# Performance work log

Measured on AMD Instinct MI355X. Metric: run time of the kernel, lower is better.

## Reference

```python
import jax, jax.numpy as jnp
import numpy as np

T, B, DG, DH, S = 48, 96, 192, 384, 3
LAM, ETA = 0.9, 0.5
LN_EPS = 1e-5

def layernorm(x, g, b):
    m = jnp.mean(x, axis=-1, keepdims=True)
    v = jnp.var(x, axis=-1, keepdims=True)
    return (x - m) * jax.lax.rsqrt(v + LN_EPS) * g + b

def setup_inputs() -> dict:
    key = jax.random.key(0)
    k0, k1, k2, k3 = jax.random.split(key, 4)
    z_seq = jax.random.normal(k0, (T, B, DG), jnp.float32)
    # kaiming-uniform-ish / xavier-ish scaling for realism
    W_h = jax.random.normal(k1, (DH, DH), jnp.float32) * (2.0 / DH) ** 0.5
    W_g = jax.random.normal(k2, (DH, DG), jnp.float32) * (1.0 / DG) ** 0.5
    b_h = jnp.zeros((DH,), jnp.float32)
    ln_g = jnp.ones((DH,), jnp.float32)
    ln_b = jnp.zeros((DH,), jnp.float32)
    alpha_fw = jax.random.uniform(k3, (1,), jnp.float32)  # cfg.alpha_fw (learned scalar)
    return dict(z_seq=z_seq, W_h=W_h, W_g=W_g, b_h=b_h, ln_g=ln_g, ln_b=ln_b, alpha_fw=alpha_fw)

def reference(z_seq, W_h, W_g, b_h, ln_g, ln_b, alpha_fw):
    # compute_k(): curvature of cosine gate
    k = jnp.where(alpha_fw >= 0,
                  1.0 + jax.nn.softplus(alpha_fw),
                  1.0 / (1.0 + jax.nn.softplus(-alpha_fw)))  # shape (1,)

    def step(carry, z_t):
        h, A = carry                                   # h: [B,DH], A: [B,DH,DH]
        h_base = h @ W_h.T + z_t @ W_g.T + b_h          # [B,DH]
        h_s = jax.nn.relu(layernorm(h_base, ln_g, ln_b))
        # inner fast-weight settling loop with cosine-similarity gate
        for _ in range(S):
            Ah = jnp.einsum('bij,bj->bi', A, h_s)       # bmm(A, h)
            dot = jnp.sum(h_s * Ah, axis=-1, keepdims=True)
            n1 = jnp.maximum(jnp.linalg.norm(h_s, axis=-1, keepdims=True), 1e-6)
            n2 = jnp.maximum(jnp.linalg.norm(Ah, axis=-1, keepdims=True), 1e-6)
            R = jnp.clip(dot / (n1 * n2), 0.0, 1.0)
            a = 1.0 - (1.0 - R) ** k                    # alpha_dyn, [B,1]
            h_s = jax.nn.relu(layernorm((1.0 - a * a) * h_base + a * Ah, ln_g, ln_b))
        h = h_s
        # Hebbian fast-weight update: A <- lambda*A + eta * h h^T
        A = LAM * A + ETA * jnp.einsum('bi,bj->bij', h, h)
        return (h, A), None

    Bn, Dh = z_seq.shape[1], W_h.shape[0]
    h0 = jnp.zeros((Bn, Dh), z_seq.dtype)
    A0 = jnp.zeros((Bn, Dh, Dh), z_seq.dtype)
    (h, A), _ = jax.lax.scan(step, (h0, A0), z_seq[:-1])

    # final (query) step: no gating, no A update, h_s = relu(LN(h_base + A h_s))
    z_t = z_seq[-1]
    h_base = h @ W_h.T + z_t @ W_g.T + b_h
    h = jax.nn.relu(layernorm(h_base, ln_g, ln_b))
    for _ in range(S):
        Ah = jnp.einsum('bij,bj->bi', A, h)
        h = jax.nn.relu(layernorm(h_base + Ah, ln_g, ln_b))
    return h
```

## Files before the change

kernel.cpp:

```cpp
#include <hip/hip_runtime.h>
#include <math.h>

#define TT    48
#define BB    96
#define DG    192
#define DH    384
#define NSTEP 47
#define SETI  3
#define NT    512
#define NWAVE 8
#define NOW   6
#define NG    32
#define RPG   12
#define LWROWS 192
#define LWSTR  97
#define PNT   256
#define PTT   24

typedef unsigned short ushort_t;
typedef float f32x2 __attribute__((ext_vector_type(2)));

template <int CTRL, int RM>
__device__ __forceinline__ float dppadd(float acc, float x) {
  int t = __builtin_amdgcn_update_dpp(0, __float_as_int(x), CTRL, RM, 0xF, false);
  return acc + __int_as_float(t);
}

__device__ __forceinline__ float row16_sum(float v) {
  v = dppadd<0x128, 0xF>(v, v);
  v = dppadd<0x124, 0xF>(v, v);
  v = dppadd<0x122, 0xF>(v, v);
  v = dppadd<0x121, 0xF>(v, v);
  return v;
}

__device__ __forceinline__ float wave_sum63(float v) {
  v = row16_sum(v);
  v = dppadd<0x142, 0xA>(v, v);
  v = dppadd<0x143, 0xC>(v, v);
  return v;
}

__device__ __forceinline__ float blo(unsigned u) {
  return __uint_as_float(u << 16);
}
__device__ __forceinline__ float bhi(unsigned u) {
  return __uint_as_float(u & 0xFFFF0000u);
}
__device__ __forceinline__ f32x2 pkfma(f32x2 a, f32x2 b, f32x2 c) {
  return __builtin_elementwise_fma(a, b, c);
}

__device__ __forceinline__ float rowdot(const uint2* w, const f32x2 (&h2)[12]) {
  f32x2 a0 = {0.f, 0.f}, a1 = {0.f, 0.f};
#pragma unroll
  for (int c = 0; c < 6; ++c) {
    uint2 u = w[c];
    a0 = pkfma(f32x2{blo(u.x), bhi(u.x)}, h2[2 * c], a0);
    a1 = pkfma(f32x2{blo(u.y), bhi(u.y)}, h2[2 * c + 1], a1);
  }
  return row16_sum((a0.x + a1.x) + (a0.y + a1.y));
}

__device__ __forceinline__ void matvec_full(
    const uint2* __restrict__ lwh, const ushort_t* __restrict__ Wh_b,
    const float* __restrict__ hs, const float* __restrict__ gzs,
    float* __restrict__ hbs, float& s1, float& s2,
    int g, int lane16, bool with_h)
{
  float rs[RPG];
  if (with_h) {
    const uint2* wsrc = (const uint2*)Wh_b;
    uint2 uw0[12];
#pragma unroll
    for (int pp = 0; pp < 2; ++pp)
#pragma unroll
      for (int c = 0; c < 6; ++c)
        uw0[pp * 6 + c] =
            wsrc[(size_t)(g + NG * (6 + pp)) * (DH / 4) + lane16 + 16 * c];
    f32x2 h2[12];
    const float4* h4 = (const float4*)hs;
#pragma unroll
    for (int c = 0; c < 6; ++c) {
      float4 hh = h4[lane16 + 16 * c];
      h2[2 * c]     = f32x2{hh.x, hh.y};
      h2[2 * c + 1] = f32x2{hh.z, hh.w};
    }
    uint2 uw1[12];
#pragma unroll
    for (int pp = 0; pp < 2; ++pp)
#pragma unroll
      for (int c = 0; c < 6; ++c)
        uw1[pp * 6 + c] =
            wsrc[(size_t)(g + NG * (8 + pp)) * (DH / 4) + lane16 + 16 * c];
#pragma unroll
    for (int p = 0; p < 6; ++p) {
      const int r = g + NG * p;
      f32x2 a0 = {0.f, 0.f}, a1 = {0.f, 0.f};
#pragma unroll
      for (int c = 0; c < 6; ++c) {
        uint2 u = lwh[r * LWSTR + lane16 + 16 * c];
        a0 = pkfma(f32x2{blo(u.x), bhi(u.x)}, h2[2 * c], a0);
        a1 = pkfma(f32x2{blo(u.y), bhi(u.y)}, h2[2 * c + 1], a1);
      }
      rs[p] = row16_sum((a0.x + a1.x) + (a0.y + a1.y));
    }
    rs[6] = rowdot(uw0, h2);
    rs[7] = rowdot(uw0 + 6, h2);
    uint2 uw2[12];
#pragma unroll
    for (int pp = 0; pp < 2; ++pp)
#pragma unroll
      for (int c = 0; c < 6; ++c)
        uw2[pp * 6 + c] =
            wsrc[(size_t)(g + NG * (10 + pp)) * (DH / 4) + lane16 + 16 * c];
    rs[8] = rowdot(uw1, h2);
    rs[9] = rowdot(uw1 + 6, h2);
    rs[10] = rowdot(uw2, h2);
    rs[11] = rowdot(uw2 + 6, h2);
  } else {
#pragma unroll
    for (int p = 0; p < RPG; ++p) rs[p] = 0.f;
  }
  if (lane16 == 0) {
#pragma unroll
    for (int p = 0; p < RPG; ++p) {
      const int r = g + NG * p;
      float vv = rs[p] + gzs[r];
      hbs[r] = vv;
      s1 += vv;
      s2 += vv * vv;
    }
  }
}

__device__ __forceinline__ void matvec_ref(
    const float* __restrict__ Wh_f, const float* __restrict__ Wg_f,
    const float* __restrict__ hs, const float* __restrict__ zsh,
    const float (&bias)[RPG], float* __restrict__ hbs,
    float& s1, float& s2, int g, int lane16, bool with_h)
{
  f32x2 h2[12];
  if (with_h) {
    const float4* h4 = (const float4*)hs;
#pragma unroll
    for (int c = 0; c < 6; ++c) {
      float4 hh = h4[lane16 + 16 * c];
      h2[2 * c]     = f32x2{hh.x, hh.y};
      h2[2 * c + 1] = f32x2{hh.z, hh.w};
    }
  }
  float4 zz[3];
  const float4* z4 = (const float4*)zsh;
#pragma unroll
  for (int c = 0; c < 3; ++c) zz[c] = z4[lane16 + 16 * c];
#pragma unroll 2
  for (int p = 0; p < RPG; ++p) {
    const int r = g + NG * p;
    f32x2 a0 = {0.f, 0.f}, a1 = {0.f, 0.f};
    const float4* wg = (const float4*)Wg_f + (size_t)r * (DG / 4);
#pragma unroll
    for (int c = 0; c < 3; ++c) {
      float4 w = wg[lane16 + 16 * c];
      a0 = pkfma(f32x2{w.x, w.y}, f32x2{zz[c].x, zz[c].y}, a0);
      a1 = pkfma(f32x2{w.z, w.w}, f32x2{zz[c].z, zz[c].w}, a1);
    }
    if (with_h) {
      const float4* wh = (const float4*)Wh_f + (size_t)r * (DH / 4);
#pragma unroll
      for (int c = 0; c < 6; ++c) {
        float4 w = wh[lane16 + 16 * c];
        a0 = pkfma(f32x2{w.x, w.y}, h2[2 * c], a0);
        a1 = pkfma(f32x2{w.z, w.w}, h2[2 * c + 1], a1);
      }
    }
    float acc = row16_sum((a0.x + a1.x) + (a0.y + a1.y));
    if (lane16 == 0) {
      float vv = acc + bias[p];
      hbs[r] = vv;
      s1 += vv;
      s2 += vv * vv;
    }
  }
}

template <bool FULL>
__global__ __launch_bounds__(NT, 2) void fw_rnn_kernel(
    const float* __restrict__ z_seq,
    const float* __restrict__ Wh_f,
    const float* __restrict__ Wg_f,
    const ushort_t* __restrict__ Wh_b,
    const float* __restrict__ gz,
    const float* __restrict__ b_h,
    const float* __restrict__ ln_g,
    const float* __restrict__ ln_b,
    const float* __restrict__ alpha_fw,
    float* __restrict__ out)
{
  __shared__ __align__(16) uint2 lwh[LWROWS * LWSTR];
  __shared__ __align__(16) float hs[DH];
  __shared__ __align__(16) float hbs[DH];
  __shared__ __align__(16) float gzs[DH];
  __shared__ __align__(16) float zsh[DG];
  __shared__ float wlam[NSTEP];
  __shared__ __align__(16) float carr[48];
  __shared__ __align__(16) float redA[NWAVE * 2];
  __shared__ __align__(16) float redB[2][32];

  const int tid    = threadIdx.x;
  const int b      = blockIdx.x;
  const int lane   = tid & 63, wv = tid >> 6;
  const int g      = tid >> 4, lane16 = tid & 15;
  const bool owner = (tid < DH);
  const bool zst   = (!FULL) && (tid >= DH) && (tid < DH + DG / 4);

  if (FULL) {
    const uint2* src = (const uint2*)Wh_b;
    for (int i = tid; i < LWROWS * 96; i += NT) {
      int row = i / 96, col = i - 96 * (i / 96);
      lwh[row * LWSTR + col] = src[(size_t)row * 96 + col];
    }
  }

  float bias[RPG];
#pragma unroll
  for (int p = 0; p < RPG; ++p) bias[p] = 0.f;
  if (!FULL && lane16 == 0) {
#pragma unroll
    for (int p = 0; p < RPG; ++p) bias[p] = b_h[g + NG * p];
  }
  float g_i = 0.f, be_i = 0.f;
  if (owner) { g_i = ln_g[tid]; be_i = ln_b[tid]; }

  const float af   = alpha_fw[0];
  const float kcur = (af >= 0.f) ? (1.f + log1pf(expf(af)))
                                 : (1.f / (1.f + log1pf(expf(-af))));
  const float invD = 1.0f / (float)DH;

  float hcol[48];
#pragma unroll
  for (int q = 0; q < 48; ++q) hcol[q] = 0.f;
  float4 hregA[6], hregB[6];
#pragma unroll
  for (int c = 0; c < 6; ++c) {
    hregA[c] = float4{0.f, 0.f, 0.f, 0.f};
    hregB[c] = float4{0.f, 0.f, 0.f, 0.f};
  }

  if (FULL && tid < DH / 4)
    ((float4*)gzs)[tid] = ((const float4*)(gz + (size_t)b * DH))[tid];
  if (!FULL && tid < DG / 4)
    ((float4*)zsh)[tid] = ((const float4*)(z_seq + (size_t)b * DG))[tid];
  if (tid < 48) carr[tid] = 0.f;
  if (tid < 2) { redB[tid][30] = 0.f; redB[tid][31] = 0.f; }
  __syncthreads();

  float Shb = 0.f, Shb2 = 0.f;

  for (int t = 0; t < NSTEP; ++t) {
    float4 gzn = {0.f, 0.f, 0.f, 0.f};
    if (FULL && tid < DH / 4)
      gzn = ((const float4*)(gz + ((size_t)(t + 1) * BB + b) * DH))[tid];

    float s1 = 0.f, s2 = 0.f;
    if (FULL)
      matvec_full(lwh, Wh_b, hs, gzs, hbs, s1, s2, g, lane16, t > 0);
    else
      matvec_ref(Wh_f, Wg_f, hs, zsh, bias, hbs, s1, s2, g, lane16, t > 0);

    if (t > 0) {
      if (g == t - 1) {
#pragma unroll
        for (int c = 0; c < 6; ++c) hregA[c] = ((const float4*)hs)[lane16 + 16 * c];
      }
      if (g + NG == t - 1) {
#pragma unroll
        for (int c = 0; c < 6; ++c) hregB[c] = ((const float4*)hs)[lane16 + 16 * c];
      }
    }
    {
      float v0 = wave_sum63(s1);
      float v1 = wave_sum63(s2);
      if (lane == 63) { redA[wv * 2] = v0; redA[wv * 2 + 1] = v1; }
    }
    __syncthreads();

    float hb = 0.f, hsv = 0.f;
    if (owner) {
      float S1 = 0.f, S2 = 0.f;
      const float4* ra4 = (const float4*)redA;
#pragma unroll
      for (int q = 0; q < 4; ++q) {
        float4 ch = ra4[q];
        S1 += ch.x + ch.z;
        S2 += ch.y + ch.w;
      }
      Shb = S1; Shb2 = S2;
      hb = hbs[tid];
      float m   = S1 * invD;
      float var = S2 * invD - m * m;
      hsv = fmaxf((hb - m) * rsqrtf(var + 1e-5f) * g_i + be_i, 0.f);
      hs[tid] = hsv;
    }
    if (t == 0) {
      if (owner) hcol[0] = hsv;
      if (tid == 0) wlam[0] = 0.5f;
      if (FULL && tid < DH / 4) ((float4*)gzs)[tid] = gzn;
      if (zst)
        ((float4*)zsh)[tid - DH] =
            ((const float4*)(z_seq + ((size_t)1 * BB + b) * DG))[tid - DH];
      __syncthreads();
      continue;
    }
    __syncthreads();

    float4 znext;
    if (zst)
      znext = ((const float4*)(z_seq + ((size_t)(t + 1) * BB + b) * DG))[tid - DH];

    for (int s = 0; s < SETI; ++s) {
      if (g < t) {
        float4 ss[6];
        const float4* s4 = (const float4*)hs;
#pragma unroll
        for (int c = 0; c < 6; ++c) ss[c] = s4[lane16 + 16 * c];
        {
          f32x2 p0 = {0.f, 0.f}, p1 = {0.f, 0.f};
#pragma unroll
          for (int c = 0; c < 6; ++c) {
            p0 = pkfma(f32x2{hregA[c].x, hregA[c].y}, f32x2{ss[c].x, ss[c].y}, p0);
            p1 = pkfma(f32x2{hregA[c].z, hregA[c].w}, f32x2{ss[c].z, ss[c].w}, p1);
          }
          float p = row16_sum((p0.x + p1.x) + (p0.y + p1.y));
          if (lane16 == 0) carr[g] = p * wlam[g];
        }
        if (g + NG < t) {
          f32x2 p0 = {0.f, 0.f}, p1 = {0.f, 0.f};
#pragma unroll
          for (int c = 0; c < 6; ++c) {
            p0 = pkfma(f32x2{hregB[c].x, hregB[c].y}, f32x2{ss[c].x, ss[c].y}, p0);
            p1 = pkfma(f32x2{hregB[c].z, hregB[c].w}, f32x2{ss[c].z, ss[c].w}, p1);
          }
          float p = row16_sum((p0.x + p1.x) + (p0.y + p1.y));
          if (lane16 == 0) carr[g + NG] = p * wlam[g + NG];
        }
      }
      __syncthreads();

      float ah = 0.f;
      if (owner) {
        const float4* c4 = (const float4*)carr;
        float a0 = 0.f, a1 = 0.f, a2 = 0.f, a3 = 0.f;
#pragma unroll
        for (int q = 0; q < 12; ++q) {
          float4 cc = c4[q];
          a0 = fmaf(cc.x, hcol[4 * q + 0], a0);
          a1 = fmaf(cc.y, hcol[4 * q + 1], a1);
          a2 = fmaf(cc.z, hcol[4 * q + 2], a2);
          a3 = fmaf(cc.w, hcol[4 * q + 3], a3);
        }
        ah = (a0 + a2) + (a1 + a3);
        float v0 = wave_sum63(hsv * ah);
        float v1 = wave_sum63(hsv * hsv);
        float v2 = wave_sum63(ah * ah);
        float v3 = wave_sum63(hb * ah);
        float v4 = wave_sum63(ah);
        if (lane == 63) {
          float* rb = redB[s & 1];
          rb[wv * 5 + 0] = v0; rb[wv * 5 + 1] = v1; rb[wv * 5 + 2] = v2;
          rb[wv * 5 + 3] = v3; rb[wv * 5 + 4] = v4;
        }
      }
      __syncthreads();

      if (owner) {
        const float4* rb4 = (const float4*)redB[s & 1];
        float S[5] = {0.f, 0.f, 0.f, 0.f, 0.f};
#pragma unroll
        for (int q = 0; q < 8; ++q) {
          float4 ch = rb4[q];
          S[(4 * q + 0) % 5] += ch.x;
          S[(4 * q + 1) % 5] += ch.y;
          S[(4 * q + 2) % 5] += ch.z;
          S[(4 * q + 3) % 5] += ch.w;
        }
        float n1 = fmaxf(sqrtf(S[1]), 1e-6f);
        float n2 = fmaxf(sqrtf(S[2]), 1e-6f);
        float R  = fminf(fmaxf(__fdividef(S[0], n1 * n2), 0.f), 1.f);
        float a  = 1.f - __expf(kcur * __logf(1.f - R));
        float beta = 1.f - a * a;
        float mu  = (beta * Shb + a * S[4]) * invD;
        float Exx = (beta * beta * Shb2 + 2.f * beta * a * S[3] + a * a * S[2]) * invD;
        float var = Exx - mu * mu;
        float xv  = beta * hb + a * ah;
        hsv = fmaxf((xv - mu) * rsqrtf(var + 1e-5f) * g_i + be_i, 0.f);
        hs[tid] = hsv;
        if (s == SETI - 1) {
#pragma unroll
          for (int q = 0; q < 48; ++q)
            if (q == t) hcol[q] = hsv;
        }
      }
      if (s == SETI - 1) {
        if (tid < t) wlam[tid] *= 0.9f;
        else if (tid == t) wlam[tid] = 0.5f;
        if (FULL && tid < DH / 4) ((float4*)gzs)[tid] = gzn;
        if (zst) ((float4*)zsh)[tid - DH] = znext;
      }
      __syncthreads();
    }
  }

  {
    float s1 = 0.f, s2 = 0.f;
    if (FULL)
      matvec_full(lwh, Wh_b, hs, gzs, hbs, s1, s2, g, lane16, true);
    else
      matvec_ref(Wh_f, Wg_f, hs, zsh, bias, hbs, s1, s2, g, lane16, true);
    if (g + NG == NSTEP - 1) {
#pragma unroll
      for (int c = 0; c < 6; ++c) hregB[c] = ((const float4*)hs)[lane16 + 16 * c];
    }
    {
      float v0 = wave_sum63(s1);
      float v1 = wave_sum63(s2);
      if (lane == 63) { redA[wv * 2] = v0; redA[wv * 2 + 1] = v1; }
    }
    __syncthreads();

    float hb = 0.f, hv = 0.f;
    if (owner) {
      float S1 = 0.f, S2 = 0.f;
      const float4* ra4 = (const float4*)redA;
#pragma unroll
      for (int q = 0; q < 4; ++q) {
        float4 ch = ra4[q];
        S1 += ch.x + ch.z;
        S2 += ch.y + ch.w;
      }
      Shb = S1; Shb2 = S2;
      hb = hbs[tid];
      float m   = S1 * invD;
      float var = S2 * invD - m * m;
      hv = fmaxf((hb - m) * rsqrtf(var + 1e-5f) * g_i + be_i, 0.f);
      hs[tid] = hv;
    }
    __syncthreads();

    for (int s = 0; s < SETI; ++s) {
      {
        float4 ss[6];
        const float4* s4 = (const float4*)hs;
#pragma unroll
        for (int c = 0; c < 6; ++c) ss[c] = s4[lane16 + 16 * c];
        {
          f32x2 p0 = {0.f, 0.f}, p1 = {0.f, 0.f};
#pragma unroll
          for (int c = 0; c < 6; ++c) {
            p0 = pkfma(f32x2{hregA[c].x, hregA[c].y}, f32x2{ss[c].x, ss[c].y}, p0);
            p1 = pkfma(f32x2{hregA[c].z, hregA[c].w}, f32x2{ss[c].z, ss[c].w}, p1);
          }
          float p = row16_sum((p0.x + p1.x) + (p0.y + p1.y));
          if (lane16 == 0) carr[g] = p * wlam[g];
        }
        if (g + NG < NSTEP) {
          f32x2 p0 = {0.f, 0.f}, p1 = {0.f, 0.f};
#pragma unroll
          for (int c = 0; c < 6; ++c) {
            p0 = pkfma(f32x2{hregB[c].x, hregB[c].y}, f32x2{ss[c].x, ss[c].y}, p0);
            p1 = pkfma(f32x2{hregB[c].z, hregB[c].w}, f32x2{ss[c].z, ss[c].w}, p1);
          }
          float p = row16_sum((p0.x + p1.x) + (p0.y + p1.y));
          if (lane16 == 0) carr[g + NG] = p * wlam[g + NG];
        }
      }
      __syncthreads();

      float ah = 0.f;
      if (owner) {
        const float4* c4 = (const float4*)carr;
        float a0 = 0.f, a1 = 0.f, a2 = 0.f, a3 = 0.f;
#pragma unroll
        for (int q = 0; q < 12; ++q) {
          float4 cc = c4[q];
          a0 = fmaf(cc.x, hcol[4 * q + 0], a0);
          a1 = fmaf(cc.y, hcol[4 * q + 1], a1);
          a2 = fmaf(cc.z, hcol[4 * q + 2], a2);
          a3 = fmaf(cc.w, hcol[4 * q + 3], a3);
        }
        ah = (a0 + a2) + (a1 + a3);
        float v0 = wave_sum63(ah);
        float v1 = wave_sum63(ah * ah);
        float v2 = wave_sum63(hb * ah);
        if (lane == 63) {
          float* rb = redB[s & 1];
          rb[wv * 5 + 0] = v0; rb[wv * 5 + 1] = v1; rb[wv * 5 + 2] = v2;
        }
      }
      __syncthreads();

      if (owner) {
        const float4* rb4 = (const float4*)redB[s & 1];
        float S[5] = {0.f, 0.f, 0.f, 0.f, 0.f};
#pragma unroll
        for (int q = 0; q < 8; ++q) {
          float4 ch = rb4[q];
          S[(4 * q + 0) % 5] += ch.x;
          S[(4 * q + 1) % 5] += ch.y;
          S[(4 * q + 2) % 5] += ch.z;
          S[(4 * q + 3) % 5] += ch.w;
        }
        float Sx  = Shb + S[0];
        float Sxx = Shb2 + 2.f * S[2] + S[1];
        float mu  = Sx * invD;
        float var = Sxx * invD - mu * mu;
        float xv  = hb + ah;
        hv = fmaxf((xv - mu) * rsqrtf(var + 1e-5f) * g_i + be_i, 0.f);
        if (s < SETI - 1) hs[tid] = hv;
      }
      if (s < SETI - 1) __syncthreads();
    }

    if (owner) out[(size_t)b * DH + tid] = hv;
  }
}

__global__ __launch_bounds__(PNT) void prep_kernel(
    const float* __restrict__ z_seq, const float* __restrict__ Wg,
    const float* __restrict__ W_h, const float* __restrict__ b_h,
    ushort_t* __restrict__ Whb, float* __restrict__ gz)
{
  __shared__ __align__(16) float zsh[PTT * DG];
  const int tid = threadIdx.x, b = blockIdx.x;
  const int t0 = blockIdx.y * PTT;
  const int g = tid >> 4, lane16 = tid & 15;

  {
    int lid = ((blockIdx.y * BB + blockIdx.x) * PNT + tid) * 3;
#pragma unroll
    for (int k = 0; k < 3; ++k) {
      int idx = lid + k;
      if (idx < DH * DH) {
        unsigned u = __float_as_uint(W_h[idx]);
        unsigned r = (u + 0x7FFFu + ((u >> 16) & 1u)) >> 16;
        Whb[idx] = (ushort_t)r;
      }
    }
  }

  for (int i = tid; i < PTT * DG / 4; i += PNT) {
    int tt = i / (DG / 4), c = i - tt * (DG / 4);
    ((float4*)zsh)[i] =
        ((const float4*)(z_seq + ((size_t)(t0 + tt) * BB + b) * DG))[c];
  }
  __syncthreads();

  for (int pp = 0; pp < 3; ++pp) {
    const int rbase = 24 * g + 8 * pp;
    float4 w[24];
#pragma unroll
    for (int j = 0; j < 8; ++j)
#pragma unroll
      for (int c = 0; c < 3; ++c)
        w[j * 3 + c] =
            ((const float4*)Wg)[(size_t)(rbase + j) * (DG / 4) + lane16 + 16 * c];
    float4 bh0 = {0.f, 0.f, 0.f, 0.f}, bh1 = {0.f, 0.f, 0.f, 0.f};
    if (lane16 == 0) {
      bh0 = ((const float4*)b_h)[rbase / 4];
      bh1 = ((const float4*)b_h)[rbase / 4 + 1];
    }
    for (int tt = 0; tt < PTT; ++tt) {
      float4 zz[3];
#pragma unroll
      for (int c = 0; c < 3; ++c)
        zz[c] = ((const float4*)zsh)[tt * (DG / 4) + lane16 + 16 * c];
      float rs[8];
#pragma unroll
      for (int j = 0; j < 8; ++j) {
        f32x2 a0 = {0.f, 0.f}, a1 = {0.f, 0.f};
#pragma unroll
        for (int c = 0; c < 3; ++c) {
          a0 = pkfma(f32x2{w[j * 3 + c].x, w[j * 3 + c].y},
                     f32x2{zz[c].x, zz[c].y}, a0);
          a1 = pkfma(f32x2{w[j * 3 + c].z, w[j * 3 + c].w},
                     f32x2{zz[c].z, zz[c].w}, a1);
        }
        rs[j] = row16_sum((a0.x + a1.x) + (a0.y + a1.y));
      }
      if (lane16 == 0) {
        float* grow = gz + ((size_t)(t0 + tt) * BB + b) * DH + rbase;
        ((float4*)grow)[0] =
            float4{rs[0] + bh0.x, rs[1] + bh0.y, rs[2] + bh0.z, rs[3] + bh0.w};
        ((float4*)grow)[1] =
            float4{rs[4] + bh1.x, rs[5] + bh1.y, rs[6] + bh1.z, rs[7] + bh1.w};
      }
    }
  }
}

extern "C" void kernel_launch(void* const* d_in, const int* in_sizes, int n_in,
                              void* d_out, int out_size, void* d_ws, size_t ws_size,
                              hipStream_t stream) {
  const float* z_seq    = (const float*)d_in[0];
  const float* W_h      = (const float*)d_in[1];
  const float* W_g      = (const float*)d_in[2];
  const float* b_h      = (const float*)d_in[3];
  const float* ln_g     = (const float*)d_in[4];
  const float* ln_b     = (const float*)d_in[5];
  const float* alpha_fw = (const float*)d_in[6];
  float* out = (float*)d_out;

  const size_t nWh = (size_t)DH * DH;
  const size_t bf16Bytes = nWh * sizeof(ushort_t);
  const size_t gzBytes   = (size_t)TT * BB * DH * sizeof(float);

  if (ws_size >= bf16Bytes + gzBytes) {
    ushort_t* Whb = (ushort_t*)d_ws;
    float* gz = (float*)((char*)d_ws + bf16Bytes);
    prep_kernel<<<dim3(BB, 2), dim3(PNT), 0, stream>>>(
        z_seq, W_g, W_h, b_h, Whb, gz);
    fw_rnn_kernel<true><<<dim3(BB), dim3(NT), 0, stream>>>(
        z_seq, W_h, W_g, Whb, gz, b_h, ln_g, ln_b, alpha_fw, out);
  } else {
    fw_rnn_kernel<false><<<dim3(BB), dim3(NT), 0, stream>>>(
        z_seq, W_h, W_g, nullptr, nullptr, b_h, ln_g, ln_b, alpha_fw, out);
  }
}
```

Measured before the change: 529.3 us.

## Recompute settled hidden state redundantly per thread to drop barriers in gate loop

Instead of having owner threads write the normalized hidden state to shared memory and then barrier, each thread group now rebuilds h_s locally from h_base, the previous Ah (stored in a new shared array), and the LN gains, using gate scalars every thread computes from the reduction buffer. This removes one __syncthreads per settling iteration plus the one after the initial layernorm. The next z load is also hoisted to the top of the step. The cost is extra redundant ALU work and shared-memory reads (hbs, ahs, ln_g, ln_b) per iteration, and more registers.

```diff
diff --git a/kernel.cpp b/kernel.cpp
--- a/kernel.cpp
+++ b/kernel.cpp
@@ -9,7 +9,6 @@
 #define SETI  3
 #define NT    512
 #define NWAVE 8
-#define NOW   6
 #define NG    32
 #define RPG   12
 #define LWROWS 192
@@ -25,7 +24,6 @@
   int t = __builtin_amdgcn_update_dpp(0, __float_as_int(x), CTRL, RM, 0xF, false);
   return acc + __int_as_float(t);
 }
-
 __device__ __forceinline__ float row16_sum(float v) {
   v = dppadd<0x128, 0xF>(v, v);
   v = dppadd<0x124, 0xF>(v, v);
@@ -33,24 +31,17 @@
   v = dppadd<0x121, 0xF>(v, v);
   return v;
 }
-
 __device__ __forceinline__ float wave_sum63(float v) {
   v = row16_sum(v);
   v = dppadd<0x142, 0xA>(v, v);
   v = dppadd<0x143, 0xC>(v, v);
   return v;
 }
-
-__device__ __forceinline__ float blo(unsigned u) {
-  return __uint_as_float(u << 16);
-}
-__device__ __forceinline__ float bhi(unsigned u) {
-  return __uint_as_float(u & 0xFFFF0000u);
-}
+__device__ __forceinline__ float blo(unsigned u) { return __uint_as_float(u << 16); }
+__device__ __forceinline__ float bhi(unsigned u) { return __uint_as_float(u & 0xFFFF0000u); }
 __device__ __forceinline__ f32x2 pkfma(f32x2 a, f32x2 b, f32x2 c) {
   return __builtin_elementwise_fma(a, b, c);
 }
-
 __device__ __forceinline__ float rowdot(const uint2* w, const f32x2 (&h2)[12]) {
   f32x2 a0 = {0.f, 0.f}, a1 = {0.f, 0.f};
 #pragma unroll
@@ -60,6 +51,31 @@
     a1 = pkfma(f32x2{blo(u.y), bhi(u.y)}, h2[2 * c + 1], a1);
   }
   return row16_sum((a0.x + a1.x) + (a0.y + a1.y));
+}
+
+__device__ __forceinline__ void gate_from(
+    const float* __restrict__ rb, float Shb, float Shb2, float kcur, float invD,
+    float& aG, float& betaG, float& muG, float& rstdG, float& S2o)
+{
+  const float4* rb4 = (const float4*)rb;
+  float S[5] = {0.f, 0.f, 0.f, 0.f, 0.f};
+#pragma unroll
+  for (int q = 0; q < 8; ++q) {
+    float4 ch = rb4[q];
+    S[(4 * q + 0) % 5] += ch.x;
+    S[(4 * q + 1) % 5] += ch.y;
+    S[(4 * q + 2) % 5] += ch.z;
+    S[(4 * q + 3) % 5] += ch.w;
+  }
+  float n1 = fmaxf(sqrtf(S[1]), 1e-6f);
+  float n2 = fmaxf(sqrtf(S[2]), 1e-6f);
+  float R  = fminf(fmaxf(__fdividef(S[0], n1 * n2), 0.f), 1.f);
+  aG   = 1.f - __expf(kcur * __logf(1.f - R));
+  betaG = 1.f - aG * aG;
+  muG  = (betaG * Shb + aG * S[4]) * invD;
+  float Exx = (betaG * betaG * Shb2 + 2.f * betaG * aG * S[3] + aG * aG * S[2]) * invD;
+  rstdG = rsqrtf(Exx - muG * muG + 1e-5f);
+  S2o = S[2];
 }
 
 __device__ __forceinline__ void matvec_full(
@@ -200,6 +216,9 @@
   __shared__ __align__(16) uint2 lwh[LWROWS * LWSTR];
   __shared__ __align__(16) float hs[DH];
   __shared__ __align__(16) float hbs[DH];
+  __shared__ __align__(16) float ahs[DH];
+  __shared__ __align__(16) float lngs[DH];
+  __shared__ __align__(16) float lnbs[DH];
   __shared__ __align__(16) float gzs[DH];
   __shared__ __align__(16) float zsh[DG];
   __shared__ float wlam[NSTEP];
@@ -230,7 +249,10 @@
     for (int p = 0; p < RPG; ++p) bias[p] = b_h[g + NG * p];
   }
   float g_i = 0.f, be_i = 0.f;
-  if (owner) { g_i = ln_g[tid]; be_i = ln_b[tid]; }
+  if (owner) {
+    g_i = ln_g[tid]; be_i = ln_b[tid];
+    lngs[tid] = g_i; lnbs[tid] = be_i;
+  }
 
   const float af   = alpha_fw[0];
   const float kcur = (af >= 0.f) ? (1.f + log1pf(expf(af)))
@@ -261,6 +283,9 @@
     float4 gzn = {0.f, 0.f, 0.f, 0.f};
     if (FULL && tid < DH / 4)
       gzn = ((const float4*)(gz + ((size_t)(t + 1) * BB + b) * DH))[tid];
+    float4 znext;
+    if (zst)
+      znext = ((const float4*)(z_seq + ((size_t)(t + 1) * BB + b) * DG))[tid - DH];
 
     float s1 = 0.f, s2 = 0.f;
     if (FULL)
@@ -285,8 +310,7 @@
     }
     __syncthreads();
 
-    float hb = 0.f, hsv = 0.f;
-    if (owner) {
+    {
       float S1 = 0.f, S2 = 0.f;
       const float4* ra4 = (const float4*)redA;
 #pragma unroll
@@ -296,40 +320,67 @@
         S2 += ch.y + ch.w;
       }
       Shb = S1; Shb2 = S2;
-      hb = hbs[tid];
-      float m   = S1 * invD;
-      float var = S2 * invD - m * m;
-      hsv = fmaxf((hb - m) * rsqrtf(var + 1e-5f) * g_i + be_i, 0.f);
-      hs[tid] = hsv;
+    }
+    const float m0    = Shb * invD;
+    const float rstd0 = rsqrtf(Shb2 * invD - m0 * m0 + 1e-5f);
+
+    float hb = 0.f, hsv = 0.f, ah = 0.f;
+    if (owner) {
+      hb  = hbs[tid];
+      hsv = fmaxf((hb - m0) * rstd0 * g_i + be_i, 0.f);
     }
     if (t == 0) {
-      if (owner) hcol[0] = hsv;
+      if (owner) { hs[tid] = hsv; hcol[0] = hsv; }
       if (tid == 0) wlam[0] = 0.5f;
       if (FULL && tid < DH / 4) ((float4*)gzs)[tid] = gzn;
-      if (zst)
-        ((float4*)zsh)[tid - DH] =
-            ((const float4*)(z_seq + ((size_t)1 * BB + b) * DG))[tid - DH];
+      if (zst) ((float4*)zsh)[tid - DH] = znext;
       __syncthreads();
       continue;
     }
-    __syncthreads();
-
-    float4 znext;
-    if (zst)
-      znext = ((const float4*)(z_seq + ((size_t)(t + 1) * BB + b) * DG))[tid - DH];
-
+
+    float aG = 0.f, betaG = 1.f, muG = m0, rstdG = rstd0, S2g = 0.f;
+#pragma unroll
     for (int s = 0; s < SETI; ++s) {
+      if (s > 0) {
+        gate_from(redB[(s - 1) & 1], Shb, Shb2, kcur, invD,
+                  aG, betaG, muG, rstdG, S2g);
+        if (owner)
+          hsv = fmaxf((betaG * hb + aG * ah - muG) * rstdG * g_i + be_i, 0.f);
+      }
       if (g < t) {
-        float4 ss[6];
-        const float4* s4 = (const float4*)hs;
-#pragma unroll
-        for (int c = 0; c < 6; ++c) ss[c] = s4[lane16 + 16 * c];
+        float4 ssv[6];
+        const float4* hb4 = (const float4*)hbs;
+        const float4* ah4 = (const float4*)ahs;
+        const float4* lg4 = (const float4*)lngs;
+        const float4* lb4 = (const float4*)lnbs;
+#pragma unroll
+        for (int c = 0; c < 6; ++c) {
+          float4 hbv = hb4[lane16 + 16 * c];
+          float4 lg  = lg4[lane16 + 16 * c];
+          float4 lb  = lb4[lane16 + 16 * c];
+          float4 x;
+          if (s == 0) {
+            x = hbv;
+          } else {
+            float4 av = ah4[lane16 + 16 * c];
+            x.x = betaG * hbv.x + aG * av.x;
+            x.y = betaG * hbv.y + aG * av.y;
+            x.z = betaG * hbv.z + aG * av.z;
+            x.w = betaG * hbv.w + aG * av.w;
+          }
+          const float mu = (s == 0) ? m0 : muG;
+          const float rs = (s == 0) ? rstd0 : rstdG;
+          ssv[c].x = fmaxf((x.x - mu) * rs * lg.x + lb.x, 0.f);
+          ssv[c].y = fmaxf((x.y - mu) * rs * lg.y + lb.y, 0.f);
+          ssv[c].z = fmaxf((x.z - mu) * rs * lg.z + lb.z, 0.f);
+          ssv[c].w = fmaxf((x.w - mu) * rs * lg.w + lb.w, 0.f);
+        }
         {
           f32x2 p0 = {0.f, 0.f}, p1 = {0.f, 0.f};
 #pragma unroll
           for (int c = 0; c < 6; ++c) {
-            p0 = pkfma(f32x2{hregA[c].x, hregA[c].y}, f32x2{ss[c].x, ss[c].y}, p0);
-            p1 = pkfma(f32x2{hregA[c].z, hregA[c].w}, f32x2{ss[c].z, ss[c].w}, p1);
+            p0 = pkfma(f32x2{hregA[c].x, hregA[c].y}, f32x2{ssv[c].x, ssv[c].y}, p0);
+            p1 = pkfma(f32x2{hregA[c].z, hregA[c].w}, f32x2{ssv[c].z, ssv[c].w}, p1);
           }
           float p = row16_sum((p0.x + p1.x) + (p0.y + p1.y));
           if (lane16 == 0) carr[g] = p * wlam[g];
@@ -338,8 +389,8 @@
           f32x2 p0 = {0.f, 0.f}, p1 = {0.f, 0.f};
 #pragma unroll
           for (int c = 0; c < 6; ++c) {
-            p0 = pkfma(f32x2{hregB[c].x, hregB[c].y}, f32x2{ss[c].x, ss[c].y}, p0);
-            p1 = pkfma(f32x2{hregB[c].z, hregB[c].w}, f32x2{ss[c].z, ss[c].w}, p1);
+            p0 = pkfma(f32x2{hregB[c].x, hregB[c].y}, f32x2{ssv[c].x, ssv[c].y}, p0);
+            p1 = pkfma(f32x2{hregB[c].z, hregB[c].w}, f32x2{ssv[c].z, ssv[c].w}, p1);
           }
           float p = row16_sum((p0.x + p1.x) + (p0.y + p1.y));
           if (lane16 == 0) carr[g + NG] = p * wlam[g + NG];
@@ -347,7 +398,6 @@
       }
       __syncthreads();
 
-      float ah = 0.f;
       if (owner) {
         const float4* c4 = (const float4*)carr;
         float a0 = 0.f, a1 = 0.f, a2 = 0.f, a3 = 0.f;
@@ -360,6 +410,7 @@
           a3 = fmaf(cc.w, hcol[4 * q + 3], a3);
         }
         ah = (a0 + a2) + (a1 + a3);
+        ahs[tid] = ah;
         float v0 = wave_sum63(hsv * ah);
         float v1 = wave_sum63(hsv * hsv);
         float v2 = wave_sum63(ah * ah);
@@ -372,43 +423,22 @@
         }
       }
       __syncthreads();
-
-      if (owner) {
-        const float4* rb4 = (const float4*)redB[s & 1];
-        float S[5] = {0.f, 0.f, 0.f, 0.f, 0.f};
-#pragma unroll
-        for (int q = 0; q < 8; ++q) {
-          float4 ch = rb4[q];
-          S[(4 * q + 0) % 5] += ch.x;
-          S[(4 * q + 1) % 5] += ch.y;
-          S[(4 * q + 2) % 5] += ch.z;
-          S[(4 * q + 3) % 5] += ch.w;
-        }
-        float n1 = fmaxf(sqrtf(S[1]), 1e-6f);
-        float n2 = fmaxf(sqrtf(S[2]), 1e-6f);
-        float R  = fminf(fmaxf(__fdividef(S[0], n1 * n2), 0.f), 1.f);
-        float a  = 1.f - __expf(kcur * __logf(1.f - R));
-        float beta = 1.f - a * a;
-        float mu  = (beta * Shb + a * S[4]) * invD;
-        float Exx = (beta * beta * Shb2 + 2.f * beta * a * S[3] + a * a * S[2]) * invD;
-        float var = Exx - mu * mu;
-        float xv  = beta * hb + a * ah;
-        hsv = fmaxf((xv - mu) * rsqrtf(var + 1e-5f) * g_i + be_i, 0.f);
-        hs[tid] = hsv;
-        if (s == SETI - 1) {
-#pragma unroll
-          for (int q = 0; q < 48; ++q)
-            if (q == t) hcol[q] = hsv;
-        }
-      }
-      if (s == SETI - 1) {
-        if (tid < t) wlam[tid] *= 0.9f;
-        else if (tid == t) wlam[tid] = 0.5f;
-        if (FULL && tid < DH / 4) ((float4*)gzs)[tid] = gzn;
-        if (zst) ((float4*)zsh)[tid - DH] = znext;
-      }
-      __syncthreads();
-    }
+    }
+
+    if (owner) {
+      gate_from(redB[(SETI - 1) & 1], Shb, Shb2, kcur, invD,
+                aG, betaG, muG, rstdG, S2g);
+      float hf = fmaxf((betaG * hb + aG * ah - muG) * rstdG * g_i + be_i, 0.f);
+      hs[tid] = hf;
+#pragma unroll
+      for (int q = 0; q < 48; ++q)
+        if (q == t) hcol[q] = hf;
+    }
+    if (tid < t) wlam[tid] *= 0.9f;
+    else if (tid == t) wlam[tid] = 0.5f;
+    if (FULL && tid < DH / 4) ((float4*)gzs)[tid] = gzn;
+    if (zst) ((float4*)zsh)[tid - DH] = znext;
+    __syncthreads();
   }
 
   {
```

After: 595.5 us. +12.5%, slower.
